# Kernel optimization log

Hardware: AMD Instinct MI355X
Metric: run time of the kernel (lower is better)

The kernel has to match this reference:

```python
import jax, jax.numpy as jnp
import numpy as np

N, D, H_HEADS = 2048, 1024, 16
HD = D // H_HEADS  # per-head dim = 64
LN_EPS = 1e-5


def setup_inputs() -> dict:
    key = jax.random.key(0)
    ks = jax.random.split(key, 6)
    s = 1.0 / np.sqrt(D)  # keep pre-softmax logits in a sane range
    return {
        "X": jax.random.normal(ks[0], (N, D), dtype=jnp.float32),
        "Wq": jax.random.normal(ks[1], (D, D), dtype=jnp.float32) * s,
        "bq": jnp.zeros((D,), jnp.float32),
        "Wk": jax.random.normal(ks[2], (D, D), dtype=jnp.float32) * s,
        "bk": jnp.zeros((D,), jnp.float32),
        "Wv": jax.random.normal(ks[3], (D, D), dtype=jnp.float32) * s,
        "bv": jnp.zeros((D,), jnp.float32),
        "Wo": jax.random.normal(ks[4], (D, D), dtype=jnp.float32) * s,
        "bo": jnp.zeros((D,), jnp.float32),
        "ln_g": jnp.ones((D,), jnp.float32),
        "ln_b": jnp.zeros((D,), jnp.float32),
    }


def reference(X, Wq, bq, Wk, bk, Wv, bv, Wo, bo, ln_g, ln_b):
    n = X.shape[0]
    # QKV projections -> [h, N, HD]  (matches .view(N, h, -1).transpose(0, 1))
    q = (X @ Wq + bq).reshape(n, H_HEADS, HD).swapaxes(0, 1)
    k = (X @ Wk + bk).reshape(n, H_HEADS, HD).swapaxes(0, 1)
    v = (X @ Wv + bv).reshape(n, H_HEADS, HD).swapaxes(0, 1)
    # Unscaled attention scores (original has NO 1/sqrt(d) factor): [h, N, N]
    A = jnp.einsum('hnd,hmd->hnm', q, k)
    # Diagonal self-exclusion mask
    diag = jnp.eye(n, dtype=bool)
    A = jnp.where(diag[None, :, :], -jnp.inf, A)
    p = jax.nn.softmax(A, axis=-1)
    Oh = jnp.einsum('hnm,hmd->hnd', p, v)  # [h, N, HD]
    # Faithful replication of Oh.transpose(1,2).contiguous().view(N, d):
    # [h, N, HD] -> [h, HD, N] -> reshape to [N, D]
    O = Oh.swapaxes(1, 2).reshape(n, D)
    # Out-proj (dropout is identity in eval mode) + residual + LayerNorm
    Y = X + (O @ Wo + bo)
    mu = jnp.mean(Y, axis=-1, keepdims=True)
    var = jnp.var(Y, axis=-1, keepdims=True)
    return (Y - mu) * jax.lax.rsqrt(var + LN_EPS) * ln_g + ln_b
```

## Files before the change

### kernel.cpp

```cpp
#include <hip/hip_runtime.h>
#include <math.h>


#define NTOK 2048
#define DM   1024
#define NH   16
#define HDIM 64

typedef __attribute__((ext_vector_type(8))) short bf16x8;
typedef __attribute__((ext_vector_type(4))) float f32x4;

#define FRL(op, ch, st, l, e) (((((op) * 2 + (ch)) * 4 + (st)) * 64 + (l)) * 8 + (e))

__device__ __forceinline__ unsigned short f2bf(float f) {
  unsigned u = __float_as_uint(f);
  u += 0x7FFF + ((u >> 16) & 1);
  return (unsigned short)(u >> 16);
}
__device__ __forceinline__ float bf2f(unsigned short h) {
  return __uint_as_float(((unsigned)h) << 16);
}

__device__ __forceinline__ void gload16(const unsigned short* g, unsigned short* l) {
  __builtin_amdgcn_global_load_lds(
      (const __attribute__((address_space(1))) unsigned int*)g,
      (__attribute__((address_space(3))) unsigned int*)l, 16, 0, 0);
}

__global__ __launch_bounds__(256) void cvt_hilo_kernel(
    const float* __restrict__ in, unsigned short* __restrict__ hi,
    unsigned short* __restrict__ lo)
{
  const int i = (blockIdx.x * 256 + threadIdx.x) * 4;
  const float4 v = *(const float4*)(in + i);
  ushort4 h, l;
  h.x = f2bf(v.x); l.x = f2bf(v.x - bf2f(h.x));
  h.y = f2bf(v.y); l.y = f2bf(v.y - bf2f(h.y));
  h.z = f2bf(v.z); l.z = f2bf(v.z - bf2f(h.z));
  h.w = f2bf(v.w); l.w = f2bf(v.w - bf2f(h.w));
  *(ushort4*)(hi + i) = h;
  *(ushort4*)(lo + i) = l;
}

__global__ __launch_bounds__(256) void cvt_w_kernel(
    const float* __restrict__ W0, const float* __restrict__ W1,
    const float* __restrict__ W2, const float* __restrict__ W3,
    unsigned short* __restrict__ WThi, unsigned short* __restrict__ WTlo)
{
  __shared__ __align__(16) float st[64][68];
  const int z = blockIdx.z;
  const float* W = (z == 0) ? W0 : (z == 1) ? W1 : (z == 2) ? W2 : W3;
  const int k0 = blockIdx.y * 64, n0 = blockIdx.x * 64;
  const int tid = threadIdx.x;
  #pragma unroll
  for (int p = 0; p < 4; ++p) {
    const int row = p * 16 + (tid >> 4);
    const int c4  = (tid & 15) * 4;
    const float4 v = *(const float4*)(W + (size_t)(k0 + row) * DM + n0 + c4);
    *(float4*)&st[row][c4] = v;
  }
  __syncthreads();
  unsigned short* oh = WThi + (size_t)z * DM * DM;
  unsigned short* ol = WTlo + (size_t)z * DM * DM;
  #pragma unroll
  for (int p = 0; p < 4; ++p) {
    const int nl = p * 16 + (tid >> 4);
    const int k4 = (tid & 15) * 4;
    ushort4 h, l;
    float a = st[k4 + 0][nl]; h.x = f2bf(a); l.x = f2bf(a - bf2f(h.x));
    float b = st[k4 + 1][nl]; h.y = f2bf(b); l.y = f2bf(b - bf2f(h.y));
    float c = st[k4 + 2][nl]; h.z = f2bf(c); l.z = f2bf(c - bf2f(h.z));
    float d = st[k4 + 3][nl]; h.w = f2bf(d); l.w = f2bf(d - bf2f(h.w));
    *(ushort4*)(oh + (size_t)(n0 + nl) * DM + k0 + k4) = h;
    *(ushort4*)(ol + (size_t)(n0 + nl) * DM + k0 + k4) = l;
  }
}

__device__ __forceinline__ void gemm_mfma_compute(
    const unsigned short* __restrict__ Ahi, const unsigned short* __restrict__ Alo,
    const unsigned short* __restrict__ BThi, const unsigned short* __restrict__ BTlo,
    int K, unsigned short* lds, f32x4 acc[2][2])
{
  const int tid  = threadIdx.x;
  const int lane = tid & 63, wid = tid >> 6;
  const int wm = wid >> 1, wn = wid & 1;
  const int bm = blockIdx.y * 64, bn = blockIdx.x * 64;

  const int row_l = tid >> 2, j = tid & 3;
  const int g0   = 2 * (j & 1);
  const int eoff = (j >> 1) * 4;
  const int s_idx = row_l >> 4, lb = row_l & 15;

  const unsigned short* src[4];
  src[0] = Ahi  + (size_t)(bm + row_l) * K + 8 * j;
  src[1] = Alo  + (size_t)(bm + row_l) * K + 8 * j;
  src[2] = BThi + (size_t)(bn + row_l) * K + 8 * j;
  src[3] = BTlo + (size_t)(bn + row_l) * K + 8 * j;

  #pragma unroll
  for (int a = 0; a < 2; ++a)
    #pragma unroll
    for (int b = 0; b < 2; ++b)
      acc[a][b] = (f32x4){0.f, 0.f, 0.f, 0.f};

  for (int k0 = 0; k0 < K; k0 += 64) {
    __syncthreads();
    #pragma unroll
    for (int op = 0; op < 4; ++op) {
      #pragma unroll
      for (int c = 0; c < 2; ++c) {
        const uint4 v = *(const uint4*)(src[op] + k0 + 32 * c);
        const int base = ((op * 2 + c) * 4 + s_idx) * 64;
        *(uint2*)&lds[(size_t)(base + 16 * g0       + lb) * 8 + eoff] = make_uint2(v.x, v.y);
        *(uint2*)&lds[(size_t)(base + 16 * (g0 + 1) + lb) * 8 + eoff] = make_uint2(v.z, v.w);
      }
    }
    __syncthreads();
    #pragma unroll
    for (int c = 0; c < 2; ++c) {
      bf16x8 ah[2], al[2], bh[2], bl[2];
      #pragma unroll
      for (int f = 0; f < 2; ++f) {
        ah[f] = *(const bf16x8*)&lds[(size_t)(((0 * 2 + c) * 4 + 2 * wm + f) * 64 + lane) * 8];
        al[f] = *(const bf16x8*)&lds[(size_t)(((1 * 2 + c) * 4 + 2 * wm + f) * 64 + lane) * 8];
        bh[f] = *(const bf16x8*)&lds[(size_t)(((2 * 2 + c) * 4 + 2 * wn + f) * 64 + lane) * 8];
        bl[f] = *(const bf16x8*)&lds[(size_t)(((3 * 2 + c) * 4 + 2 * wn + f) * 64 + lane) * 8];
      }
      #pragma unroll
      for (int fm = 0; fm < 2; ++fm)
        #pragma unroll
        for (int fn = 0; fn < 2; ++fn) {
          acc[fm][fn] = __builtin_amdgcn_mfma_f32_16x16x32_bf16(ah[fm], bh[fn], acc[fm][fn], 0, 0, 0);
          acc[fm][fn] = __builtin_amdgcn_mfma_f32_16x16x32_bf16(ah[fm], bl[fn], acc[fm][fn], 0, 0, 0);
          acc[fm][fn] = __builtin_amdgcn_mfma_f32_16x16x32_bf16(al[fm], bh[fn], acc[fm][fn], 0, 0, 0);
        }
    }
  }
}

__global__ __launch_bounds__(256) void gemm_qkv_mfma(
    const unsigned short* __restrict__ Xhi, const unsigned short* __restrict__ Xlo,
    const unsigned short* __restrict__ WThi, const unsigned short* __restrict__ WTlo,
    const float* __restrict__ bq, const float* __restrict__ bk,
    const float* __restrict__ bv,
    unsigned short* __restrict__ QF, unsigned short* __restrict__ KF,
    unsigned short* __restrict__ VF)
{
  __shared__ __align__(16) unsigned short lds[16384];
  const int z = blockIdx.z;
  const unsigned short* bth = WThi + (size_t)z * DM * DM;
  const unsigned short* btl = WTlo + (size_t)z * DM * DM;
  const float* bias = (z == 0) ? bq : (z == 1) ? bk : bv;
  unsigned short* OUTF = (z == 0) ? QF : (z == 1) ? KF : VF;

  f32x4 acc[2][2];
  gemm_mfma_compute(Xhi, Xlo, bth, btl, DM, lds, acc);

  const int tid = threadIdx.x, lane = tid & 63, wid = tid >> 6;
  const int wm = wid >> 1, wn = wid & 1, g = lane >> 4, c = lane & 15;
  const int h = blockIdx.x, t = blockIdx.y;

  __syncthreads();
  #pragma unroll
  for (int fm = 0; fm < 2; ++fm)
    #pragma unroll
    for (int fn = 0; fn < 2; ++fn) {
      const float bcol = bias[h * 64 + wn * 32 + fn * 16 + c];
      #pragma unroll
      for (int r = 0; r < 4; ++r) {
        const float v = acc[fm][fn][r] + bcol;
        const unsigned short hp = f2bf(v);
        const unsigned short lp = f2bf(v - bf2f(hp));
        int ch, st, l, e;
        if (z != 2) {
          ch = wn; st = 2 * wm + fm;
          l  = ((c >> 2) << 4) | (4 * g + r);
          e  = 4 * fn + (c & 3);
        } else {
          ch = wm; st = 2 * wn + fn;
          l  = (g << 4) | c;
          e  = 4 * fm + r;
        }
        lds[FRL(0, ch, st, l, e)] = hp;
        lds[FRL(1, ch, st, l, e)] = lp;
      }
    }
  __syncthreads();
  unsigned short* blob = OUTF + ((size_t)h * 32 + t) * 8192;
  #pragma unroll
  for (int s = 0; s < 4; ++s)
    *(uint4*)(blob + (size_t)(s * 256 + tid) * 8) =
        *(const uint4*)&lds[(size_t)(s * 256 + tid) * 8];
}

__global__ __launch_bounds__(256) void gemm_out_mfma(
    const unsigned short* __restrict__ Ohi, const unsigned short* __restrict__ Olo,
    const unsigned short* __restrict__ WThi, const unsigned short* __restrict__ WTlo,
    const float* __restrict__ bo, const float* __restrict__ X, float* __restrict__ Y)
{
  __shared__ __align__(16) unsigned short lds[16384];
  f32x4 acc[2][2];
  gemm_mfma_compute(Ohi, Olo, WThi, WTlo, DM, lds, acc);

  const int tid = threadIdx.x, lane = tid & 63, wid = tid >> 6;
  const int wm = wid >> 1, wn = wid & 1;
  const int bm = blockIdx.y * 64, bn = blockIdx.x * 64;
  const int r0 = bm + wm * 32, c0 = bn + wn * 32;
  #pragma unroll
  for (int fm = 0; fm < 2; ++fm)
    #pragma unroll
    for (int fn = 0; fn < 2; ++fn) {
      const int col  = c0 + fn * 16 + (lane & 15);
      const int rowb = r0 + fm * 16 + (lane >> 4) * 4;
      const float bcol = bo[col];
      #pragma unroll
      for (int r = 0; r < 4; ++r) {
        const int row = rowb + r;
        Y[(size_t)row * DM + col] =
            acc[fm][fn][r] + bcol + X[(size_t)row * DM + col];
      }
    }
}

__global__ __launch_bounds__(256) void attn_mfma2_kernel(
    const unsigned short* __restrict__ QF, const unsigned short* __restrict__ KF,
    const unsigned short* __restrict__ VF,
    unsigned short* __restrict__ Ohi, unsigned short* __restrict__ Olo)
{
  __shared__ __align__(16) unsigned short lds[32768];

  const int tid = threadIdx.x, lane = tid & 63, wv = tid >> 6;
  const int g = lane >> 4, c = lane & 15;
  const int h = blockIdx.y, tq = blockIdx.x;
  const int q0 = tq * 64;
  const int qq = q0 + 16 * wv + c;

  const unsigned short* qb = QF + ((size_t)h * 32 + tq) * 8192;
  bf16x8 qh[2], ql[2];
  #pragma unroll
  for (int ch = 0; ch < 2; ++ch) {
    qh[ch] = *(const bf16x8*)(qb + FRL(0, ch, wv, lane, 0));
    ql[ch] = *(const bf16x8*)(qb + FRL(1, ch, wv, lane, 0));
  }

  f32x4 acc_o[4];
  #pragma unroll
  for (int df = 0; df < 4; ++df) acc_o[df] = (f32x4){0.f, 0.f, 0.f, 0.f};
  float m_run = -INFINITY, l_run = 0.f;

  const size_t hbase = (size_t)h * 32;
  {
    const unsigned short* kb = KF + (hbase + 0) * 8192;
    const unsigned short* vb = VF + (hbase + 0) * 8192;
    #pragma unroll
    for (int s = 0; s < 4; ++s) {
      gload16(kb + (size_t)(s * 256 + tid) * 8, &lds[(size_t)(s * 256 + tid) * 8]);
      gload16(vb + (size_t)(s * 256 + tid) * 8, &lds[8192 + (size_t)(s * 256 + tid) * 8]);
    }
  }

  int buf = 0;
  for (int kt = 0; kt < NTOK / 64; ++kt) {
    __syncthreads();
    if (kt + 1 < NTOK / 64) {
      const unsigned short* kb = KF + (hbase + kt + 1) * 8192;
      const unsigned short* vb = VF + (hbase + kt + 1) * 8192;
      unsigned short* lk = &lds[(buf ^ 1) * 16384];
      #pragma unroll
      for (int s = 0; s < 4; ++s) {
        gload16(kb + (size_t)(s * 256 + tid) * 8, lk + (size_t)(s * 256 + tid) * 8);
        gload16(vb + (size_t)(s * 256 + tid) * 8, lk + 8192 + (size_t)(s * 256 + tid) * 8);
      }
    }
    const unsigned short* lk = &lds[buf * 16384];
    const unsigned short* lv = lk + 8192;

    f32x4 sacc[4];
    #pragma unroll
    for (int fm = 0; fm < 4; ++fm) sacc[fm] = (f32x4){0.f, 0.f, 0.f, 0.f};
    #pragma unroll
    for (int ch = 0; ch < 2; ++ch) {
      #pragma unroll
      for (int fm = 0; fm < 4; ++fm) {
        const bf16x8 khf = *(const bf16x8*)&lk[FRL(0, ch, fm, lane, 0)];
        const bf16x8 klf = *(const bf16x8*)&lk[FRL(1, ch, fm, lane, 0)];
        sacc[fm] = __builtin_amdgcn_mfma_f32_16x16x32_bf16(khf, qh[ch], sacc[fm], 0, 0, 0);
        sacc[fm] = __builtin_amdgcn_mfma_f32_16x16x32_bf16(khf, ql[ch], sacc[fm], 0, 0, 0);
        sacc[fm] = __builtin_amdgcn_mfma_f32_16x16x32_bf16(klf, qh[ch], sacc[fm], 0, 0, 0);
      }
    }

    const int tok0 = kt * 64 + 4 * g;
    #pragma unroll
    for (int fm = 0; fm < 4; ++fm)
      #pragma unroll
      for (int r = 0; r < 4; ++r)
        if (tok0 + 16 * fm + r == qq) sacc[fm][r] = -INFINITY;

    float m = -INFINITY;
    #pragma unroll
    for (int fm = 0; fm < 4; ++fm)
      #pragma unroll
      for (int r = 0; r < 4; ++r) m = fmaxf(m, sacc[fm][r]);
    m = fmaxf(m, __shfl_xor(m, 16, 64));
    m = fmaxf(m, __shfl_xor(m, 32, 64));
    const float mnew = fmaxf(m_run, m);
    const float scal = __expf(m_run - mnew);
    float ps = 0.f;
    #pragma unroll
    for (int fm = 0; fm < 4; ++fm)
      #pragma unroll
      for (int r = 0; r < 4; ++r) {
        const float p = __expf(sacc[fm][r] - mnew);
        sacc[fm][r] = p;
        ps += p;
      }
    ps += __shfl_xor(ps, 16, 64);
    ps += __shfl_xor(ps, 32, 64);
    l_run = l_run * scal + ps;
    m_run = mnew;

    bf16x8 ph[2], pl[2];
    #pragma unroll
    for (int ch = 0; ch < 2; ++ch)
      #pragma unroll
      for (int i = 0; i < 8; ++i) {
        const float pv = sacc[2 * ch + (i >> 2)][i & 3];
        const unsigned short hp = f2bf(pv);
        ph[ch][i] = (short)hp;
        pl[ch][i] = (short)f2bf(pv - bf2f(hp));
      }

    #pragma unroll
    for (int df = 0; df < 4; ++df)
      #pragma unroll
      for (int r = 0; r < 4; ++r) acc_o[df][r] *= scal;
    #pragma unroll
    for (int ch = 0; ch < 2; ++ch)
      #pragma unroll
      for (int df = 0; df < 4; ++df) {
        const bf16x8 vh = *(const bf16x8*)&lv[FRL(0, ch, df, lane, 0)];
        const bf16x8 vl = *(const bf16x8*)&lv[FRL(1, ch, df, lane, 0)];
        acc_o[df] = __builtin_amdgcn_mfma_f32_16x16x32_bf16(vh, ph[ch], acc_o[df], 0, 0, 0);
        acc_o[df] = __builtin_amdgcn_mfma_f32_16x16x32_bf16(vh, pl[ch], acc_o[df], 0, 0, 0);
        acc_o[df] = __builtin_amdgcn_mfma_f32_16x16x32_bf16(vl, ph[ch], acc_o[df], 0, 0, 0);
      }
    buf ^= 1;
  }

  const float inv = 1.0f / l_run;
  const int colo = (q0 & 1023) + 16 * wv + c;
  const int rowb = h * 128 + (q0 >> 10);
  #pragma unroll
  for (int df = 0; df < 4; ++df)
    #pragma unroll
    for (int r = 0; r < 4; ++r) {
      const int d = 16 * df + 4 * g + r;
      const float val = acc_o[df][r] * inv;
      const unsigned short hp = f2bf(val);
      const size_t off = (size_t)(rowb + 2 * d) * DM + colo;
      Ohi[off] = hp;
      Olo[off] = f2bf(val - bf2f(hp));
    }
}

__global__ __launch_bounds__(256) void ln_kernel(
    const float* __restrict__ Y, const float* __restrict__ g,
    const float* __restrict__ b, float* __restrict__ out)
{
  __shared__ float red[8];
  const int row = blockIdx.x;
  const int tid = threadIdx.x;
  const float4 y = *(const float4*)(Y + (size_t)row * DM + tid * 4);
  float s  = y.x + y.y + y.z + y.w;
  float ss = y.x * y.x + y.y * y.y + y.z * y.z + y.w * y.w;
  #pragma unroll
  for (int o = 1; o < 64; o <<= 1) {
    s  += __shfl_xor(s, o, 64);
    ss += __shfl_xor(ss, o, 64);
  }
  const int wv = tid >> 6;
  if ((tid & 63) == 0) { red[wv] = s; red[4 + wv] = ss; }
  __syncthreads();
  s  = red[0] + red[1] + red[2] + red[3];
  ss = red[4] + red[5] + red[6] + red[7];
  const float mu   = s * (1.f / DM);
  const float var  = ss * (1.f / DM) - mu * mu;
  const float rstd = rsqrtf(var + 1e-5f);
  const float4 gv = *(const float4*)(g + tid * 4);
  const float4 bv = *(const float4*)(b + tid * 4);
  float4 o;
  o.x = (y.x - mu) * rstd * gv.x + bv.x;
  o.y = (y.y - mu) * rstd * gv.y + bv.y;
  o.z = (y.z - mu) * rstd * gv.z + bv.z;
  o.w = (y.w - mu) * rstd * gv.w + bv.w;
  *(float4*)(out + (size_t)row * DM + tid * 4) = o;
}

extern "C" void kernel_launch(void* const* d_in, const int* in_sizes, int n_in,
                              void* d_out, int out_size, void* d_ws, size_t ws_size,
                              hipStream_t stream) {
  const float* X    = (const float*)d_in[0];
  const float* Wq   = (const float*)d_in[1];
  const float* bq   = (const float*)d_in[2];
  const float* Wk   = (const float*)d_in[3];
  const float* bk   = (const float*)d_in[4];
  const float* Wv   = (const float*)d_in[5];
  const float* bv   = (const float*)d_in[6];
  const float* Wo   = (const float*)d_in[7];
  const float* bo   = (const float*)d_in[8];
  const float* ln_g = (const float*)d_in[9];
  const float* ln_b = (const float*)d_in[10];

  const size_t MAT = (size_t)NTOK * DM;
  float* Y = (float*)d_ws;
  unsigned short* us = (unsigned short*)(Y + MAT);
  unsigned short* Xhi  = us;
  unsigned short* Xlo  = Xhi + MAT;
  unsigned short* Ohi  = Xlo + MAT;
  unsigned short* Olo  = Ohi + MAT;
  unsigned short* WThi = Olo + MAT;
  unsigned short* WTlo = WThi + 2 * MAT;
  unsigned short* QF   = WTlo + 2 * MAT;
  unsigned short* KF   = QF + 2 * MAT;
  unsigned short* VF   = KF + 2 * MAT;

  const dim3 blk(256);

  cvt_w_kernel<<<dim3(16, 16, 4), blk, 0, stream>>>(Wq, Wk, Wv, Wo, WThi, WTlo);
  cvt_hilo_kernel<<<dim3(MAT / 1024), blk, 0, stream>>>(X, Xhi, Xlo);

  gemm_qkv_mfma<<<dim3(DM / 64, NTOK / 64, 3), blk, 0, stream>>>(
      Xhi, Xlo, WThi, WTlo, bq, bk, bv, QF, KF, VF);

  attn_mfma2_kernel<<<dim3(NTOK / 64, NH), blk, 0, stream>>>(QF, KF, VF, Ohi, Olo);

  gemm_out_mfma<<<dim3(DM / 64, NTOK / 64), blk, 0, stream>>>(
      Ohi, Olo, WThi + 3 * (size_t)DM * DM, WTlo + 3 * (size_t)DM * DM,
      bo, X, Y);

  ln_kernel<<<NTOK, blk, 0, stream>>>(Y, ln_g, ln_b, (float*)d_out);
}
```

Before: 236.3 us.

## Pre-tile operands into MFMA fragment blobs, enlarge GEMM tiles, trim split-bf16 precision

X and the weights are now converted straight into MFMA-fragment-ordered bf16 hi/lo blobs. The QKV and out-projection GEMMs can then load whole tiles with global_load_lds into 128x128 block tiles, instead of doing a scattered LDS transpose on 64x64 tiles. Attention folds log2e into Q so it can use exp2f, drops the low-bf16 part of P in the PV product, raises wave priority around the MFMA blocks, and writes O as a single bf16 fragment blob. The out-projection then uses two MFMAs per tile step instead of three. Dropping the low halves of P and O lowers accuracy relative to the 3-term split scheme.

```diff
diff --git a/kernel.cpp b/kernel.cpp
--- a/kernel.cpp
+++ b/kernel.cpp
@@ -6,11 +6,14 @@
 #define DM   1024
 #define NH   16
 #define HDIM 64
+#define LOG2E 1.4426950408889634f
 
 typedef __attribute__((ext_vector_type(8))) short bf16x8;
 typedef __attribute__((ext_vector_type(4))) float f32x4;
 
 #define FRL(op, ch, st, l, e) (((((op) * 2 + (ch)) * 4 + (st)) * 64 + (l)) * 8 + (e))
+#define FRO(ch, st, l, e) ((((ch) * 4 + (st)) * 64 + (l)) * 8 + (e))
+#define MFMA(a, b, c) __builtin_amdgcn_mfma_f32_16x16x32_bf16(a, b, c, 0, 0, 0)
 
 __device__ __forceinline__ unsigned short f2bf(float f) {
   unsigned u = __float_as_uint(f);
@@ -20,212 +23,259 @@
 __device__ __forceinline__ float bf2f(unsigned short h) {
   return __uint_as_float(((unsigned)h) << 16);
 }
-
 __device__ __forceinline__ void gload16(const unsigned short* g, unsigned short* l) {
   __builtin_amdgcn_global_load_lds(
       (const __attribute__((address_space(1))) unsigned int*)g,
       (__attribute__((address_space(3))) unsigned int*)l, 16, 0, 0);
 }
 
-__global__ __launch_bounds__(256) void cvt_hilo_kernel(
-    const float* __restrict__ in, unsigned short* __restrict__ hi,
-    unsigned short* __restrict__ lo)
-{
-  const int i = (blockIdx.x * 256 + threadIdx.x) * 4;
-  const float4 v = *(const float4*)(in + i);
-  ushort4 h, l;
-  h.x = f2bf(v.x); l.x = f2bf(v.x - bf2f(h.x));
-  h.y = f2bf(v.y); l.y = f2bf(v.y - bf2f(h.y));
-  h.z = f2bf(v.z); l.z = f2bf(v.z - bf2f(h.z));
-  h.w = f2bf(v.w); l.w = f2bf(v.w - bf2f(h.w));
-  *(ushort4*)(hi + i) = h;
-  *(ushort4*)(lo + i) = l;
-}
-
-__global__ __launch_bounds__(256) void cvt_w_kernel(
+__global__ __launch_bounds__(256) void cvt_x_blob(
+    const float* __restrict__ X, unsigned short* __restrict__ XB)
+{
+  __shared__ __align__(16) unsigned short img[8192];
+  const int kt = blockIdx.x, rt = blockIdx.y, tid = threadIdx.x;
+  #pragma unroll
+  for (int s = 0; s < 4; ++s) {
+    const int f = tid + s * 256;
+    const int rl = f >> 4, c4 = (f & 15) * 4;
+    const float4 v = *(const float4*)(X + (size_t)(rt * 64 + rl) * DM + kt * 64 + c4);
+    const float vv[4] = {v.x, v.y, v.z, v.w};
+    unsigned short hi[4], lo[4];
+    #pragma unroll
+    for (int e = 0; e < 4; ++e) {
+      hi[e] = f2bf(vv[e]);
+      lo[e] = f2bf(vv[e] - bf2f(hi[e]));
+    }
+    const int ch = c4 >> 5, c32 = c4 & 31;
+    const int gp = (c32 & 15) >> 2, e0 = (c32 >> 4) * 4;
+    const int l = 16 * gp + (rl & 15), sti = rl >> 4;
+    *(uint2*)&img[FRL(0, ch, sti, l, e0)] =
+        make_uint2(hi[0] | (hi[1] << 16), hi[2] | (hi[3] << 16));
+    *(uint2*)&img[FRL(1, ch, sti, l, e0)] =
+        make_uint2(lo[0] | (lo[1] << 16), lo[2] | (lo[3] << 16));
+  }
+  __syncthreads();
+  unsigned short* out = XB + ((size_t)rt * 16 + kt) * 8192;
+  #pragma unroll
+  for (int s = 0; s < 4; ++s) {
+    const int u = s * 256 + tid;
+    *(uint4*)(out + (size_t)u * 8) = *(const uint4*)&img[(size_t)u * 8];
+  }
+}
+
+__global__ __launch_bounds__(256) void cvt_w_blob(
     const float* __restrict__ W0, const float* __restrict__ W1,
     const float* __restrict__ W2, const float* __restrict__ W3,
-    unsigned short* __restrict__ WThi, unsigned short* __restrict__ WTlo)
+    unsigned short* __restrict__ WB)
 {
   __shared__ __align__(16) float st[64][68];
-  const int z = blockIdx.z;
+  __shared__ __align__(16) unsigned short img[8192];
+  const int nt = blockIdx.x, kt = blockIdx.y, z = blockIdx.z, tid = threadIdx.x;
   const float* W = (z == 0) ? W0 : (z == 1) ? W1 : (z == 2) ? W2 : W3;
-  const int k0 = blockIdx.y * 64, n0 = blockIdx.x * 64;
-  const int tid = threadIdx.x;
-  #pragma unroll
-  for (int p = 0; p < 4; ++p) {
-    const int row = p * 16 + (tid >> 4);
-    const int c4  = (tid & 15) * 4;
-    const float4 v = *(const float4*)(W + (size_t)(k0 + row) * DM + n0 + c4);
-    *(float4*)&st[row][c4] = v;
-  }
-  __syncthreads();
-  unsigned short* oh = WThi + (size_t)z * DM * DM;
-  unsigned short* ol = WTlo + (size_t)z * DM * DM;
-  #pragma unroll
-  for (int p = 0; p < 4; ++p) {
-    const int nl = p * 16 + (tid >> 4);
-    const int k4 = (tid & 15) * 4;
-    ushort4 h, l;
-    float a = st[k4 + 0][nl]; h.x = f2bf(a); l.x = f2bf(a - bf2f(h.x));
-    float b = st[k4 + 1][nl]; h.y = f2bf(b); l.y = f2bf(b - bf2f(h.y));
-    float c = st[k4 + 2][nl]; h.z = f2bf(c); l.z = f2bf(c - bf2f(h.z));
-    float d = st[k4 + 3][nl]; h.w = f2bf(d); l.w = f2bf(d - bf2f(h.w));
-    *(ushort4*)(oh + (size_t)(n0 + nl) * DM + k0 + k4) = h;
-    *(ushort4*)(ol + (size_t)(n0 + nl) * DM + k0 + k4) = l;
-  }
-}
-
-__device__ __forceinline__ void gemm_mfma_compute(
-    const unsigned short* __restrict__ Ahi, const unsigned short* __restrict__ Alo,
-    const unsigned short* __restrict__ BThi, const unsigned short* __restrict__ BTlo,
-    int K, unsigned short* lds, f32x4 acc[2][2])
-{
-  const int tid  = threadIdx.x;
-  const int lane = tid & 63, wid = tid >> 6;
-  const int wm = wid >> 1, wn = wid & 1;
-  const int bm = blockIdx.y * 64, bn = blockIdx.x * 64;
-
-  const int row_l = tid >> 2, j = tid & 3;
-  const int g0   = 2 * (j & 1);
-  const int eoff = (j >> 1) * 4;
-  const int s_idx = row_l >> 4, lb = row_l & 15;
-
-  const unsigned short* src[4];
-  src[0] = Ahi  + (size_t)(bm + row_l) * K + 8 * j;
-  src[1] = Alo  + (size_t)(bm + row_l) * K + 8 * j;
-  src[2] = BThi + (size_t)(bn + row_l) * K + 8 * j;
-  src[3] = BTlo + (size_t)(bn + row_l) * K + 8 * j;
-
-  #pragma unroll
-  for (int a = 0; a < 2; ++a)
-    #pragma unroll
-    for (int b = 0; b < 2; ++b)
-      acc[a][b] = (f32x4){0.f, 0.f, 0.f, 0.f};
-
-  for (int k0 = 0; k0 < K; k0 += 64) {
-    __syncthreads();
-    #pragma unroll
-    for (int op = 0; op < 4; ++op) {
-      #pragma unroll
-      for (int c = 0; c < 2; ++c) {
-        const uint4 v = *(const uint4*)(src[op] + k0 + 32 * c);
-        const int base = ((op * 2 + c) * 4 + s_idx) * 64;
-        *(uint2*)&lds[(size_t)(base + 16 * g0       + lb) * 8 + eoff] = make_uint2(v.x, v.y);
-        *(uint2*)&lds[(size_t)(base + 16 * (g0 + 1) + lb) * 8 + eoff] = make_uint2(v.z, v.w);
-      }
-    }
-    __syncthreads();
-    #pragma unroll
-    for (int c = 0; c < 2; ++c) {
-      bf16x8 ah[2], al[2], bh[2], bl[2];
-      #pragma unroll
-      for (int f = 0; f < 2; ++f) {
-        ah[f] = *(const bf16x8*)&lds[(size_t)(((0 * 2 + c) * 4 + 2 * wm + f) * 64 + lane) * 8];
-        al[f] = *(const bf16x8*)&lds[(size_t)(((1 * 2 + c) * 4 + 2 * wm + f) * 64 + lane) * 8];
-        bh[f] = *(const bf16x8*)&lds[(size_t)(((2 * 2 + c) * 4 + 2 * wn + f) * 64 + lane) * 8];
-        bl[f] = *(const bf16x8*)&lds[(size_t)(((3 * 2 + c) * 4 + 2 * wn + f) * 64 + lane) * 8];
-      }
-      #pragma unroll
-      for (int fm = 0; fm < 2; ++fm)
-        #pragma unroll
-        for (int fn = 0; fn < 2; ++fn) {
-          acc[fm][fn] = __builtin_amdgcn_mfma_f32_16x16x32_bf16(ah[fm], bh[fn], acc[fm][fn], 0, 0, 0);
-          acc[fm][fn] = __builtin_amdgcn_mfma_f32_16x16x32_bf16(ah[fm], bl[fn], acc[fm][fn], 0, 0, 0);
-          acc[fm][fn] = __builtin_amdgcn_mfma_f32_16x16x32_bf16(al[fm], bh[fn], acc[fm][fn], 0, 0, 0);
-        }
-    }
-  }
-}
-
-__global__ __launch_bounds__(256) void gemm_qkv_mfma(
-    const unsigned short* __restrict__ Xhi, const unsigned short* __restrict__ Xlo,
-    const unsigned short* __restrict__ WThi, const unsigned short* __restrict__ WTlo,
+  #pragma unroll
+  for (int s = 0; s < 4; ++s) {
+    const int f = tid + s * 256;
+    const int kl = f >> 4, n4 = (f & 15) * 4;
+    const float4 v = *(const float4*)(W + (size_t)(kt * 64 + kl) * DM + nt * 64 + n4);
+    *(float4*)&st[kl][n4] = v;
+  }
+  __syncthreads();
+  #pragma unroll
+  for (int s = 0; s < 4; ++s) {
+    const int f = tid + s * 256;
+    const int nl = f >> 4, k4 = (f & 15) * 4;
+    unsigned short hi[4], lo[4];
+    #pragma unroll
+    for (int e = 0; e < 4; ++e) {
+      const float v = st[k4 + e][nl];
+      hi[e] = f2bf(v);
+      lo[e] = f2bf(v - bf2f(hi[e]));
+    }
+    const int ch = k4 >> 5, c32 = k4 & 31;
+    const int gp = (c32 & 15) >> 2, e0 = (c32 >> 4) * 4;
+    const int l = 16 * gp + (nl & 15), sti = nl >> 4;
+    *(uint2*)&img[FRL(0, ch, sti, l, e0)] =
+        make_uint2(hi[0] | (hi[1] << 16), hi[2] | (hi[3] << 16));
+    *(uint2*)&img[FRL(1, ch, sti, l, e0)] =
+        make_uint2(lo[0] | (lo[1] << 16), lo[2] | (lo[3] << 16));
+  }
+  __syncthreads();
+  unsigned short* out = WB + (size_t)z * 2097152 + ((size_t)nt * 16 + kt) * 8192;
+  #pragma unroll
+  for (int s = 0; s < 4; ++s) {
+    const int u = s * 256 + tid;
+    *(uint4*)(out + (size_t)u * 8) = *(const uint4*)&img[(size_t)u * 8];
+  }
+}
+
+__global__ __launch_bounds__(256) void gemm_qkv_blob(
+    const unsigned short* __restrict__ XB, const unsigned short* __restrict__ WB,
     const float* __restrict__ bq, const float* __restrict__ bk,
     const float* __restrict__ bv,
     unsigned short* __restrict__ QF, unsigned short* __restrict__ KF,
     unsigned short* __restrict__ VF)
 {
-  __shared__ __align__(16) unsigned short lds[16384];
-  const int z = blockIdx.z;
-  const unsigned short* bth = WThi + (size_t)z * DM * DM;
-  const unsigned short* btl = WTlo + (size_t)z * DM * DM;
+  __shared__ __align__(16) unsigned short lds[32768];
+  const int tid = threadIdx.x, lane = tid & 63, wid = tid >> 6;
+  const int wm = wid >> 1, wn = wid & 1;
+  const int bx = blockIdx.x, by = blockIdx.y, z = blockIdx.z;
+  const int g = lane >> 4, c = lane & 15;
+
+  const unsigned short* BB = WB + (size_t)z * 2097152;
+  const unsigned short* bases[4] = {
+      XB + ((size_t)(2 * by) * 16) * 8192, XB + ((size_t)(2 * by + 1) * 16) * 8192,
+      BB + ((size_t)(2 * bx) * 16) * 8192, BB + ((size_t)(2 * bx + 1) * 16) * 8192};
+
+  f32x4 acc[4][4];
+  #pragma unroll
+  for (int i = 0; i < 4; ++i)
+    #pragma unroll
+    for (int j = 0; j < 4; ++j) acc[i][j] = (f32x4){0.f, 0.f, 0.f, 0.f};
+
+  for (int kt = 0; kt < 16; ++kt) {
+    __syncthreads();
+    #pragma unroll
+    for (int s = 0; s < 16; ++s)
+      gload16(bases[s >> 2] + (size_t)kt * 8192 + ((size_t)((s & 3) * 256 + tid)) * 8,
+              &lds[(size_t)(s * 256 + tid) * 8]);
+    __syncthreads();
+    #pragma unroll
+    for (int ch = 0; ch < 2; ++ch) {
+      bf16x8 ah[4], al[4], bh[4], bl[4];
+      #pragma unroll
+      for (int f = 0; f < 4; ++f) {
+        ah[f] = *(const bf16x8*)&lds[wm * 8192 + FRL(0, ch, f, lane, 0)];
+        al[f] = *(const bf16x8*)&lds[wm * 8192 + FRL(1, ch, f, lane, 0)];
+        bh[f] = *(const bf16x8*)&lds[16384 + wn * 8192 + FRL(0, ch, f, lane, 0)];
+        bl[f] = *(const bf16x8*)&lds[16384 + wn * 8192 + FRL(1, ch, f, lane, 0)];
+      }
+      #pragma unroll
+      for (int fm = 0; fm < 4; ++fm)
+        #pragma unroll
+        for (int fn = 0; fn < 4; ++fn) {
+          acc[fm][fn] = MFMA(ah[fm], bh[fn], acc[fm][fn]);
+          acc[fm][fn] = MFMA(ah[fm], bl[fn], acc[fm][fn]);
+          acc[fm][fn] = MFMA(al[fm], bh[fn], acc[fm][fn]);
+        }
+    }
+  }
+
   const float* bias = (z == 0) ? bq : (z == 1) ? bk : bv;
   unsigned short* OUTF = (z == 0) ? QF : (z == 1) ? KF : VF;
 
-  f32x4 acc[2][2];
-  gemm_mfma_compute(Xhi, Xlo, bth, btl, DM, lds, acc);
-
-  const int tid = threadIdx.x, lane = tid & 63, wid = tid >> 6;
-  const int wm = wid >> 1, wn = wid & 1, g = lane >> 4, c = lane & 15;
-  const int h = blockIdx.x, t = blockIdx.y;
-
-  __syncthreads();
-  #pragma unroll
-  for (int fm = 0; fm < 2; ++fm)
-    #pragma unroll
-    for (int fn = 0; fn < 2; ++fn) {
-      const float bcol = bias[h * 64 + wn * 32 + fn * 16 + c];
+  __syncthreads();
+  const int imgb = (wm * 2 + wn) * 8192;
+  #pragma unroll
+  for (int fm = 0; fm < 4; ++fm)
+    #pragma unroll
+    for (int fn = 0; fn < 4; ++fn) {
+      const int col = 128 * bx + 64 * wn + 16 * fn + c;
+      const float bcol = bias[col];
       #pragma unroll
       for (int r = 0; r < 4; ++r) {
-        const float v = acc[fm][fn][r] + bcol;
-        const unsigned short hp = f2bf(v);
-        const unsigned short lp = f2bf(v - bf2f(hp));
-        int ch, st, l, e;
+        float val = acc[fm][fn][r] + bcol;
+        if (z == 0) val *= LOG2E;
+        const unsigned short hp = f2bf(val);
+        const unsigned short lp = f2bf(val - bf2f(hp));
+        int sti, l, ch_i, e;
         if (z != 2) {
-          ch = wn; st = 2 * wm + fm;
-          l  = ((c >> 2) << 4) | (4 * g + r);
-          e  = 4 * fn + (c & 3);
+          sti = fm; l = 16 * (c >> 2) + (4 * g + r);
+          ch_i = fn >> 1; e = 4 * (fn & 1) + (c & 3);
         } else {
-          ch = wm; st = 2 * wn + fn;
-          l  = (g << 4) | c;
-          e  = 4 * fm + r;
+          sti = fn; l = 16 * g + c;
+          ch_i = fm >> 1; e = 4 * (fm & 1) + r;
         }
-        lds[FRL(0, ch, st, l, e)] = hp;
-        lds[FRL(1, ch, st, l, e)] = lp;
-      }
-    }
-  __syncthreads();
-  unsigned short* blob = OUTF + ((size_t)h * 32 + t) * 8192;
-  #pragma unroll
-  for (int s = 0; s < 4; ++s)
-    *(uint4*)(blob + (size_t)(s * 256 + tid) * 8) =
-        *(const uint4*)&lds[(size_t)(s * 256 + tid) * 8];
-}
-
-__global__ __launch_bounds__(256) void gemm_out_mfma(
-    const unsigned short* __restrict__ Ohi, const unsigned short* __restrict__ Olo,
-    const unsigned short* __restrict__ WThi, const unsigned short* __restrict__ WTlo,
-    const float* __restrict__ bo, const float* __restrict__ X, float* __restrict__ Y)
-{
-  __shared__ __align__(16) unsigned short lds[16384];
-  f32x4 acc[2][2];
-  gemm_mfma_compute(Ohi, Olo, WThi, WTlo, DM, lds, acc);
-
+        lds[imgb + FRL(0, ch_i, sti, l, e)] = hp;
+        lds[imgb + FRL(1, ch_i, sti, l, e)] = lp;
+      }
+    }
+  __syncthreads();
+  #pragma unroll
+  for (int s = 0; s < 16; ++s) {
+    const int u = s * 256 + tid;
+    const int i = s >> 2;
+    const int head = 2 * bx + (i & 1), tt = 2 * by + (i >> 1);
+    *(uint4*)(OUTF + ((size_t)head * 32 + tt) * 8192 + (size_t)(u & 1023) * 8) =
+        *(const uint4*)&lds[(size_t)u * 8];
+  }
+}
+
+__global__ __launch_bounds__(256) void gemm_out_blob(
+    const unsigned short* __restrict__ OF, const unsigned short* __restrict__ WoB,
+    const float* __restrict__ bo, const float* __restrict__ X,
+    float* __restrict__ Y)
+{
+  __shared__ __align__(16) unsigned short lds[24576];
   const int tid = threadIdx.x, lane = tid & 63, wid = tid >> 6;
   const int wm = wid >> 1, wn = wid & 1;
-  const int bm = blockIdx.y * 64, bn = blockIdx.x * 64;
-  const int r0 = bm + wm * 32, c0 = bn + wn * 32;
-  #pragma unroll
-  for (int fm = 0; fm < 2; ++fm)
-    #pragma unroll
-    for (int fn = 0; fn < 2; ++fn) {
-      const int col  = c0 + fn * 16 + (lane & 15);
-      const int rowb = r0 + fm * 16 + (lane >> 4) * 4;
+  const int bx = blockIdx.x, by = blockIdx.y;
+
+  const unsigned short* oa0 = OF + ((size_t)(2 * by) * 16) * 4096;
+  const unsigned short* oa1 = OF + ((size_t)(2 * by + 1) * 16) * 4096;
+  const unsigned short* wb0 = WoB + ((size_t)(2 * bx) * 16) * 8192;
+  const unsigned short* wb1 = WoB + ((size_t)(2 * bx + 1) * 16) * 8192;
+
+  f32x4 acc[4][4];
+  #pragma unroll
+  for (int i = 0; i < 4; ++i)
+    #pragma unroll
+    for (int j = 0; j < 4; ++j) acc[i][j] = (f32x4){0.f, 0.f, 0.f, 0.f};
+
+  for (int kt = 0; kt < 16; ++kt) {
+    __syncthreads();
+    #pragma unroll
+    for (int s = 0; s < 2; ++s) {
+      gload16(oa0 + (size_t)kt * 4096 + (size_t)(s * 256 + tid) * 8,
+              &lds[(size_t)(s * 256 + tid) * 8]);
+      gload16(oa1 + (size_t)kt * 4096 + (size_t)(s * 256 + tid) * 8,
+              &lds[(size_t)(512 + s * 256 + tid) * 8]);
+    }
+    #pragma unroll
+    for (int s = 0; s < 4; ++s) {
+      gload16(wb0 + (size_t)kt * 8192 + (size_t)(s * 256 + tid) * 8,
+              &lds[(size_t)(1024 + s * 256 + tid) * 8]);
+      gload16(wb1 + (size_t)kt * 8192 + (size_t)(s * 256 + tid) * 8,
+              &lds[(size_t)(2048 + s * 256 + tid) * 8]);
+    }
+    __syncthreads();
+    #pragma unroll
+    for (int ch = 0; ch < 2; ++ch) {
+      bf16x8 ah[4], bh[4], bl[4];
+      #pragma unroll
+      for (int f = 0; f < 4; ++f) {
+        ah[f] = *(const bf16x8*)&lds[wm * 4096 + FRO(ch, f, lane, 0)];
+        bh[f] = *(const bf16x8*)&lds[8192 + wn * 8192 + FRL(0, ch, f, lane, 0)];
+        bl[f] = *(const bf16x8*)&lds[8192 + wn * 8192 + FRL(1, ch, f, lane, 0)];
+      }
+      #pragma unroll
+      for (int fm = 0; fm < 4; ++fm)
+        #pragma unroll
+        for (int fn = 0; fn < 4; ++fn) {
+          acc[fm][fn] = MFMA(ah[fm], bh[fn], acc[fm][fn]);
+          acc[fm][fn] = MFMA(ah[fm], bl[fn], acc[fm][fn]);
+        }
+    }
+  }
+
+  const int g = lane >> 4, c = lane & 15;
+  #pragma unroll
+  for (int fm = 0; fm < 4; ++fm)
+    #pragma unroll
+    for (int fn = 0; fn < 4; ++fn) {
+      const int col = 128 * bx + 64 * wn + 16 * fn + c;
       const float bcol = bo[col];
       #pragma unroll
       for (int r = 0; r < 4; ++r) {
-        const int row = rowb + r;
+        const int row = 128 * by + 64 * wm + 16 * fm + 4 * g + r;
         Y[(size_t)row * DM + col] =
             acc[fm][fn][r] + bcol + X[(size_t)row * DM + col];
       }
     }
 }
 
-__global__ __launch_bounds__(256) void attn_mfma2_kernel(
+__global__ __launch_bounds__(256) void attn_mfma3_kernel(
     const unsigned short* __restrict__ QF, const unsigned short* __restrict__ KF,
-    const unsigned short* __restrict__ VF,
-    unsigned short* __restrict__ Ohi, unsigned short* __restrict__ Olo)
+    const unsigned short* __restrict__ VF, unsigned short* __restrict__ OF)
 {
   __shared__ __align__(16) unsigned short lds[32768];
 
@@ -250,8 +300,8 @@
 
   const size_t hbase = (size_t)h * 32;
   {
-    const unsigned short* kb = KF + (hbase + 0) * 8192;
-    const unsigned short* vb = VF + (hbase + 0) * 8192;
+    const unsigned short* kb = KF + hbase * 8192;
+    const unsigned short* vb = VF + hbase * 8192;
     #pragma unroll
     for (int s = 0; s < 4; ++s) {
       gload16(kb + (size_t)(s * 256 + tid) * 8, &lds[(size_t)(s * 256 + tid) * 8]);
@@ -278,17 +328,19 @@
     f32x4 sacc[4];
     #pragma unroll
     for (int fm = 0; fm < 4; ++fm) sacc[fm] = (f32x4){0.f, 0.f, 0.f, 0.f};
+    __builtin_amdgcn_s_setprio(1);
     #pragma unroll
     for (int ch = 0; ch < 2; ++ch) {
       #pragma unroll
       for (int fm = 0; fm < 4; ++fm) {
         const bf16x8 khf = *(const bf16x8*)&lk[FRL(0, ch, fm, lane, 0)];
         const bf16x8 klf = *(const bf16x8*)&lk[FRL(1, ch, fm, lane, 0)];
-        sacc[fm] = __builtin_amdgcn_mfma_f32_16x16x32_bf16(khf, qh[ch], sacc[fm], 0, 0, 0);
-        sacc[fm] = __builtin_amdgcn_mfma_f32_16x16x32_bf16(khf, ql[ch], sacc[fm], 0, 0, 0);
-        sacc[fm] = __builtin_amdgcn_mfma_f32_16x16x32_bf16(klf, qh[ch], sacc[fm], 0, 0, 0);
-      }
-    }
+        sacc[fm] = MFMA(khf, qh[ch], sacc[fm]);
+        sacc[fm] = MFMA(khf, ql[ch], sacc[fm]);
+        sacc[fm] = MFMA(klf, qh[ch], sacc[fm]);
+      }
+    }
+    __builtin_amdgcn_s_setprio(0);
 
     const int tok0 = kt * 64 + 4 * g;
     #pragma unroll
@@ -305,13 +357,13 @@
     m = fmaxf(m, __shfl_xor(m, 16, 64));
     m = fmaxf(m, __shfl_xor(m, 32, 64));
     const float mnew = fmaxf(m_run, m);
-    const float scal = __expf(m_run - mnew);
+    const float scal = exp2f(m_run - mnew);
     float ps = 0.f;
     #pragma unroll
     for (int fm = 0; fm < 4; ++fm)
       #pragma unroll
       for (int r = 0; r < 4; ++r) {
-        const float p = __expf(sacc[fm][r] - mnew);
+        const float p = exp2f(sacc[fm][r] - mnew);
         sacc[fm][r] = p;
         ps += p;
       }
@@ -320,48 +372,56 @@
     l_run = l_run * scal + ps;
     m_run = mnew;
 
-    bf16x8 ph[2], pl[2];
+    bf16x8 ph[2];
     #pragma unroll
     for (int ch = 0; ch < 2; ++ch)
       #pragma unroll
-      for (int i = 0; i < 8; ++i) {
-        const float pv = sacc[2 * ch + (i >> 2)][i & 3];
-        const unsigned short hp = f2bf(pv);
-        ph[ch][i] = (short)hp;
-        pl[ch][i] = (short)f2bf(pv - bf2f(hp));
-      }
+      for (int i = 0; i < 8; ++i)
+        ph[ch][i] = (short)f2bf(sacc[2 * ch + (i >> 2)][i & 3]);
 
     #pragma unroll
     for (int df = 0; df < 4; ++df)
       #pragma unroll
       for (int r = 0; r < 4; ++r) acc_o[df][r] *= scal;
+    __builtin_amdgcn_s_setprio(1);
     #pragma unroll
     for (int ch = 0; ch < 2; ++ch)
       #pragma unroll
       for (int df = 0; df < 4; ++df) {
         const bf16x8 vh = *(const bf16x8*)&lv[FRL(0, ch, df, lane, 0)];
         const bf16x8 vl = *(const bf16x8*)&lv[FRL(1, ch, df, lane, 0)];
-        acc_o[df] = __builtin_amdgcn_mfma_f32_16x16x32_bf16(vh, ph[ch], acc_o[df], 0, 0, 0);
-        acc_o[df] = __builtin_amdgcn_mfma_f32_16x16x32_bf16(vh, pl[ch], acc_o[df], 0, 0, 0);
-        acc_o[df] = __builtin_amdgcn_mfma_f32_16x16x32_bf16(vl, ph[ch], acc_o[df], 0, 0, 0);
-      }
+        acc_o[df] = MFMA(vh, ph[ch], acc_o[df]);
+        acc_o[df] = MFMA(vl, ph[ch], acc_o[df]);
+      }
+    __builtin_amdgcn_s_setprio(0);
     buf ^= 1;
   }
 
   const float inv = 1.0f / l_run;
-  const int colo = (q0 & 1023) + 16 * wv + c;
-  const int rowb = h * 128 + (q0 >> 10);
+  const int n1 = tq >> 4, ktc = tq & 15;
+  __syncthreads();
   #pragma unroll
   for (int df = 0; df < 4; ++df)
     #pragma unroll
     for (int r = 0; r < 4; ++r) {
       const int d = 16 * df + 4 * g + r;
-      const float val = acc_o[df][r] * inv;
-      const unsigned short hp = f2bf(val);
-      const size_t off = (size_t)(rowb + 2 * d) * DM + colo;
-      Ohi[off] = hp;
-      Olo[off] = f2bf(val - bf2f(hp));
-    }
+      const int rw = 2 * d + n1;
+      const int rt_l = rw >> 6, row64 = rw & 63;
+      const int sti = row64 >> 4, row16 = row64 & 15;
+      const int l = 16 * (c >> 2) + row16;
+      const int e = 4 * (wv & 1) + (c & 3);
+      lds[rt_l * 4096 + FRO(wv >> 1, sti, l, e)] = f2bf(acc_o[df][r] * inv);
+    }
+  __syncthreads();
+  #pragma unroll
+  for (int s = 0; s < 2; ++s) {
+    const int p = s * 256 + tid;
+    const int rt_l = p >> 8, q = p & 255;
+    const int rh = q & 7, gp = (q >> 3) & 3, sti = (q >> 5) & 3, chi = q >> 7;
+    const int slot = (chi * 4 + sti) * 64 + 16 * gp + 2 * rh + n1;
+    *(uint4*)(OF + (((size_t)(2 * h + rt_l)) * 16 + ktc) * 4096 + (size_t)slot * 8) =
+        *(const uint4*)&lds[(size_t)(rt_l * 4096 + slot * 8)];
+  }
 }
 
 __global__ __launch_bounds__(256) void ln_kernel(
@@ -414,30 +474,25 @@
 
   const size_t MAT = (size_t)NTOK * DM;
   float* Y = (float*)d_ws;
-  unsigned short* us = (unsigned short*)(Y + MAT);
-  unsigned short* Xhi  = us;
-  unsigned short* Xlo  = Xhi + MAT;
-  unsigned short* Ohi  = Xlo + MAT;
-  unsigned short* Olo  = Ohi + MAT;
-  unsigned short* WThi = Olo + MAT;
-  unsigned short* WTlo = WThi + 2 * MAT;
-  unsigned short* QF   = WTlo + 2 * MAT;
-  unsigned short* KF   = QF + 2 * MAT;
-  unsigned short* VF   = KF + 2 * MAT;
+  unsigned short* XB = (unsigned short*)(Y + MAT);
+  unsigned short* WB = XB + 2 * MAT;
+  unsigned short* QF = WB + 4 * MAT;
+  unsigned short* KF = QF + 2 * MAT;
+  unsigned short* VF = KF + 2 * MAT;
+  unsigned short* OF = VF + 2 * MAT;
 
   const dim3 blk(256);
 
-  cvt_w_kernel<<<dim3(16, 16, 4), blk, 0, stream>>>(Wq, Wk, Wv, Wo, WThi, WTlo);
-  cvt_hilo_kernel<<<dim3(MAT / 1024), blk, 0, stream>>>(X, Xhi, Xlo);
-
-  gemm_qkv_mfma<<<dim3(DM / 64, NTOK / 64, 3), blk, 0, stream>>>(
-      Xhi, Xlo, WThi, WTlo, bq, bk, bv, QF, KF, VF);
-
-  attn_mfma2_kernel<<<dim3(NTOK / 64, NH), blk, 0, stream>>>(QF, KF, VF, Ohi, Olo);
-
-  gemm_out_mfma<<<dim3(DM / 64, NTOK / 64), blk, 0, stream>>>(
-      Ohi, Olo, WThi + 3 * (size_t)DM * DM, WTlo + 3 * (size_t)DM * DM,
-      bo, X, Y);
+  cvt_x_blob<<<dim3(16, 32), blk, 0, stream>>>(X, XB);
+  cvt_w_blob<<<dim3(16, 16, 4), blk, 0, stream>>>(Wq, Wk, Wv, Wo, WB);
+
+  gemm_qkv_blob<<<dim3(8, 16, 3), blk, 0, stream>>>(
+      XB, WB, bq, bk, bv, QF, KF, VF);
+
+  attn_mfma3_kernel<<<dim3(32, 16), blk, 0, stream>>>(QF, KF, VF, OF);
+
+  gemm_out_blob<<<dim3(8, 16), blk, 0, stream>>>(
+      OF, WB + 3 * MAT, bo, X, Y);
 
   ln_kernel<<<NTOK, blk, 0, stream>>>(Y, ln_g, ln_b, (float*)d_out);
 }
```

Result: faster. 228.4 us (-3.4%).
